# Kernel tuning notes

Measured on AMD Instinct MI355X. Metric: run time of the kernel, lower is better.

The kernel has to match this reference:

```python
import jax, jax.numpy as jnp
import numpy as np

# dims
N_USER = 30000; N_ITEM = 30000; HID = 256; HEADS = 4; DH = HID // HEADS
L = 2; E_BUYS = 200000
IMG_D = 512; TASTE_D = 768; NUTR_D = 20; LR = 64; IMG_RANK = 64
EPS = 1e-5
# node type order: 0=user 1=item 2=taste 3=intention 4=image
# edge type order: taste->item, intention->item, image->item, user->item (buys), item->user (bought_by)


def _bn(x, g, b):
    # nn.BatchNorm1d in training mode (biased variance), deterministic
    mu = jnp.mean(x, axis=0)
    var = jnp.mean((x - mu) ** 2, axis=0)
    return (x - mu) * jax.lax.rsqrt(var + EPS) * g + b


def _segment_softmax(logits, seg, n):
    m = jax.ops.segment_max(logits, seg, num_segments=n)
    m = jnp.where(jnp.isfinite(m), m, 0.0)
    e = jnp.exp(logits - m[seg])
    s = jax.ops.segment_sum(e, seg, num_segments=n)
    return e / (s[seg] + 1e-16)


def _model(p, user_id, item_id, buys_src, buys_dst):
    # --- encoders (dropout = identity in eval) ---
    xu = jax.nn.relu(_bn(p['user_emb'][user_id] @ p['user_W'] + p['user_b'], p['user_bn_g'], p['user_bn_b']))
    xi = jax.nn.relu(_bn(p['item_emb'][item_id] @ p['item_W'] + p['item_b'], p['item_bn_g'], p['item_bn_b']))
    ximg = (p['image_feat'] @ p['img_U']) @ p['img_V'] + p['img_b']  # LowRankLinear
    xt = p['taste_feat'] @ p['taste_W'] + p['taste_b']
    xn = p['intent_feat'] @ p['intent_W'] + p['intent_b']
    xs = [xu, xi, xt, xn, ximg]
    assoc = jnp.arange(N_ITEM, dtype=jnp.int32)
    # (src_type, dst_type, src_idx, dst_idx)
    edges = [(2, 1, assoc, assoc), (3, 1, assoc, assoc), (4, 1, assoc, assoc),
             (0, 1, buys_src, buys_dst), (1, 0, buys_dst, buys_src)]
    scale = 1.0 / np.sqrt(DH)
    n_of = [N_USER, N_ITEM]
    for l in range(L):
        k, q, v = [], [], []
        for t in range(5):
            kqv = xs[t] @ p['kqv_W'][l, t] + p['kqv_b'][l, t]
            kk, qq, vv = jnp.split(kqv, 3, axis=1)
            k.append(kk.reshape(-1, HEADS, DH))
            q.append(qq.reshape(-1, HEADS, DH))
            v.append(vv.reshape(-1, HEADS, DH))
        buf = {0: [], 1: []}
        for e, (s, d, si, di) in enumerate(edges):
            # relation-specific per-head transforms of source k/v (all src nodes, then gather)
            ke = jnp.einsum('nhd,hde->nhe', k[s], p['k_rel'][l, e])
            ve = jnp.einsum('nhd,hde->nhe', v[s], p['v_rel'][l, e])
            logit = jnp.sum(q[d][di] * ke[si], axis=-1) * p['p_rel'][l, e] * scale  # [E,H]
            buf[d].append((logit, ve[si], di))
        new_xs = list(xs)
        for d in (0, 1):  # dst node types: user, item
            logits = jnp.concatenate([b[0] for b in buf[d]], axis=0)
            msgs = jnp.concatenate([b[1] for b in buf[d]], axis=0)
            dsts = jnp.concatenate([b[2] for b in buf[d]], axis=0)
            alpha = _segment_softmax(logits, dsts, n_of[d])  # softmax over ALL incoming edges per dst node
            agg = jax.ops.segment_sum(alpha[:, :, None] * msgs, dsts, num_segments=n_of[d])
            o = jax.nn.gelu(agg.reshape(-1, HID), approximate=False) @ p['out_W'][l, d] + p['out_b'][l, d]
            sg = jax.nn.sigmoid(p['skip'][l, d])
            o = sg * o + (1.0 - sg) * xs[d]  # HGTConv learned skip
            o = o + xs[d]                    # MultiModalFusionGAT residual
            o = jax.nn.relu(_bn(o, p['fbn_g'][l, d], p['fbn_b'][l, d]))  # per-type BN+ReLU (dropout eval)
            new_xs[d] = o
        xs = new_xs  # taste/intention/image pass through unchanged
    return jnp.stack(xs, axis=0)  # [5, 30000, HID]


def setup_inputs():
    key = jax.random.key(0)
    ks = iter(jax.random.split(key, 48))
    def nrm(shape, scale=0.05):
        return jax.random.normal(next(ks), shape, dtype=jnp.float32) * scale
    z = lambda *s: jnp.zeros(s, jnp.float32)
    o = lambda *s: jnp.ones(s, jnp.float32)
    inp = {}
    inp['user_id'] = jnp.arange(N_USER, dtype=jnp.int32)
    inp['item_id'] = jnp.arange(N_ITEM, dtype=jnp.int32)
    inp['buys_src'] = jax.random.randint(next(ks), (E_BUYS,), 0, N_USER, dtype=jnp.int32)
    inp['buys_dst'] = jax.random.randint(next(ks), (E_BUYS,), 0, N_ITEM, dtype=jnp.int32)
    inp['image_feat'] = nrm((N_ITEM, IMG_D), 1.0)
    inp['taste_feat'] = nrm((N_ITEM, TASTE_D), 1.0)
    inp['intent_feat'] = nrm((N_ITEM, NUTR_D), 1.0)
    inp['user_emb'] = nrm((N_USER, LR), 0.1)
    inp['user_W'] = nrm((LR, HID)); inp['user_b'] = z(HID)
    inp['user_bn_g'] = o(HID); inp['user_bn_b'] = z(HID)
    inp['item_emb'] = nrm((N_ITEM, LR), 0.1)
    inp['item_W'] = nrm((LR, HID)); inp['item_b'] = z(HID)
    inp['item_bn_g'] = o(HID); inp['item_bn_b'] = z(HID)
    inp['img_U'] = nrm((IMG_D, IMG_RANK)); inp['img_V'] = nrm((IMG_RANK, HID)); inp['img_b'] = z(HID)
    inp['taste_W'] = nrm((TASTE_D, HID)); inp['taste_b'] = z(HID)
    inp['intent_W'] = nrm((NUTR_D, HID)); inp['intent_b'] = z(HID)
    inp['kqv_W'] = nrm((L, 5, HID, 3 * HID)); inp['kqv_b'] = z(L, 5, 3 * HID)
    inp['out_W'] = nrm((L, 5, HID, HID)); inp['out_b'] = z(L, 5, HID)
    inp['k_rel'] = nrm((L, 5, HEADS, DH, DH))
    inp['v_rel'] = nrm((L, 5, HEADS, DH, DH))
    inp['p_rel'] = o(L, 5, HEADS)
    inp['skip'] = o(L, 5)
    inp['fbn_g'] = o(L, 2, HID); inp['fbn_b'] = z(L, 2, HID)
    return inp


def reference(user_id, item_id, buys_src, buys_dst, image_feat, taste_feat, intent_feat,
              user_emb, user_W, user_b, user_bn_g, user_bn_b,
              item_emb, item_W, item_b, item_bn_g, item_bn_b,
              img_U, img_V, img_b, taste_W, taste_b, intent_W, intent_b,
              kqv_W, kqv_b, out_W, out_b, k_rel, v_rel, p_rel, skip, fbn_g, fbn_b):
    p = dict(image_feat=image_feat, taste_feat=taste_feat, intent_feat=intent_feat,
             user_emb=user_emb, user_W=user_W, user_b=user_b, user_bn_g=user_bn_g, user_bn_b=user_bn_b,
             item_emb=item_emb, item_W=item_W, item_b=item_b, item_bn_g=item_bn_g, item_bn_b=item_bn_b,
             img_U=img_U, img_V=img_V, img_b=img_b, taste_W=taste_W, taste_b=taste_b,
             intent_W=intent_W, intent_b=intent_b, kqv_W=kqv_W, kqv_b=kqv_b, out_W=out_W, out_b=out_b,
             k_rel=k_rel, v_rel=v_rel, p_rel=p_rel, skip=skip, fbn_g=fbn_g, fbn_b=fbn_b)
    return _model(p, user_id, item_id, buys_src, buys_dst)
```

## Files before the change

kernel.cpp:

```cpp
#include <hip/hip_runtime.h>
#include <math.h>

#define HID 256
#define EBUY 200000
#define NNODE 30000
#define MPD 30208
static const size_t S  = (size_t)NNODE * HID;
static const size_t SP = (size_t)MPD * HID;

typedef __attribute__((ext_vector_type(8))) short  short8;
typedef __attribute__((ext_vector_type(4))) float  f32x4;

#define OFF_TASTE 0
#define OFF_INT   196608
#define OFF_IMGU  204800
#define OFF_IMGV  237568
#define OFF_USER  253952
#define OFF_ITEM  270336
#define OFF_OUTW  286720
#define WENC_TOT  548864

__device__ __forceinline__ float gelu_f(float x) {
    return 0.5f * x * (1.0f + erff(x * 0.70710678118654752f));
}
__device__ __forceinline__ unsigned short f2bf(float f) {
    unsigned u = __float_as_uint(f);
    u = (u + 0x7FFFu + ((u >> 16) & 1u)) >> 16;
    return (unsigned short)u;
}
__device__ __forceinline__ float b2f(unsigned short us) {
    return __uint_as_float((unsigned)us << 16);
}
__device__ __forceinline__ void gl_lds16(const unsigned short* g, unsigned short* l) {
    __builtin_amdgcn_global_load_lds(
        (const __attribute__((address_space(1))) unsigned int*)g,
        (__attribute__((address_space(3))) unsigned int*)l, 16, 0, 0);
}
__device__ __forceinline__ int xcd_swz(int bid, int nwg) {
    int q = nwg >> 3, r = nwg & 7;
    int xc = bid & 7, i = bid >> 3;
    int base = (xc < r) ? xc * (q + 1) : r * (q + 1) + (xc - r) * q;
    return base + i;
}

__global__ void conv_pad(const float* __restrict__ in, unsigned short* __restrict__ o,
                         int M, int K, int Kpad)
{
    int i = blockIdx.x * 256 + threadIdx.x;
    if (i >= M * Kpad) return;
    int r = i / Kpad, k = i % Kpad;
    o[i] = (k < K) ? f2bf(in[(size_t)r * K + k]) : (unsigned short)0;
}

__global__ void wtconv_all(const float* __restrict__ taste_W, const float* __restrict__ intent_W,
                           const float* __restrict__ img_U, const float* __restrict__ img_V,
                           const float* __restrict__ user_W, const float* __restrict__ item_W,
                           const float* __restrict__ out_W, unsigned short* __restrict__ WENC)
{
    int i = blockIdx.x * 256 + threadIdx.x;
    if (i >= WENC_TOT) return;
    const float* W; int K, N, Kpad, idx;
    if (i < OFF_INT)        { W = taste_W;  K = 768; N = 256; Kpad = 768; idx = i - OFF_TASTE; }
    else if (i < OFF_IMGU)  { W = intent_W; K = 20;  N = 256; Kpad = 32;  idx = i - OFF_INT; }
    else if (i < OFF_IMGV)  { W = img_U;    K = 512; N = 64;  Kpad = 512; idx = i - OFF_IMGU; }
    else if (i < OFF_USER)  { W = img_V;    K = 64;  N = 256; Kpad = 64;  idx = i - OFF_IMGV; }
    else if (i < OFF_ITEM)  { W = user_W;   K = 64;  N = 256; Kpad = 64;  idx = i - OFF_USER; }
    else if (i < OFF_OUTW)  { W = item_W;   K = 64;  N = 256; Kpad = 64;  idx = i - OFF_ITEM; }
    else {
        int k = (i - OFF_OUTW) >> 16;
        int l = k >> 1, d = k & 1;
        W = out_W + (size_t)(l * 5 + d) * 65536;
        K = 256; N = 256; Kpad = 256; idx = (i - OFF_OUTW) & 65535;
    }
    int n = idx / Kpad, kk = idx % Kpad;
    WENC[i] = (kk < K) ? f2bf(W[(size_t)kk * N + n]) : (unsigned short)0;
}

__global__ void build_kqv(const float* __restrict__ kqv_W, const float* __restrict__ kqv_b,
                          const float* __restrict__ k_rel, const float* __restrict__ v_rel,
                          unsigned short* __restrict__ WALL, float* __restrict__ bALL)
{
    int s = blockIdx.y;
    int l = s / 5, t = s % 5;
    static const int es[5] = {3, 4, 0, 1, 2};
    int e = es[t];
    int tid = blockIdx.x * 256 + threadIdx.x;
    if (tid >= 257 * 768) return;
    int r = tid / 768, c = tid % 768;
    int cb = c >> 8, cc = c & 255;
    int h = cc >> 6, dd = cc & 63;
    const float* W = kqv_W + (size_t)s * 196608;
    const float* bv = kqv_b + (size_t)s * 768;
    const float* Wrow = (r < 256) ? (W + (size_t)r * 768) : bv;
    if (cb == 1) {
        if (t >= 2) return;
        float outv = Wrow[256 + cc];
        if (r < 256) WALL[(size_t)s * 196608 + (size_t)(512 + cc) * 256 + r] = f2bf(outv);
        else         bALL[s * 768 + 512 + cc] = outv;
        return;
    }
    const float* R = ((cb == 0) ? k_rel : v_rel) + (size_t)(l * 5 + e) * 16384 + (size_t)h * 4096;
    int sb = (cb == 0) ? 0 : 512;
    float sum = 0.f;
    #pragma unroll 8
    for (int d = 0; d < 64; ++d)
        sum += Wrow[sb + h * 64 + d] * R[d * 64 + dd];
    int col = (cb == 0) ? cc : 256 + cc;
    if (r < 256) WALL[(size_t)s * 196608 + (size_t)col * 256 + r] = f2bf(sum);
    else         bALL[s * 768 + col] = sum;
}

template<int AF32, int GATH2, int BSEL, int EPI>
__launch_bounds__(256)
__global__ void gemm_mfma(const void* __restrict__ Ap, const void* __restrict__ Ap2,
                          const int* __restrict__ g1, const int* __restrict__ g2,
                          const unsigned short* __restrict__ BT0, int bStride,
                          const float* __restrict__ bias0, const float* __restrict__ bias1,
                          int biasStride,
                          float* __restrict__ D0, unsigned short* __restrict__ Db,
                          unsigned short* __restrict__ Db2,
                          int M, int N, int K)
{
    __shared__ union {
        unsigned short AB[4][4096];
        unsigned short O[16384];
    } sm;
    const int tid = threadIdx.x;
    const int gx = gridDim.x;
    int bid = xcd_swz(blockIdx.y * gx + blockIdx.x, gx * gridDim.y);
    const int bx = bid % gx, by = bid / gx;
    const int row0 = by * 128, col0 = bx * 128;
    const int wid = tid >> 6, lane = tid & 63;
    const int wr = wid >> 1, wc = wid & 1;
    const int l16 = lane & 15, kg = lane >> 4;
    const int tt = (BSEL || GATH2) ? (by / 236) : 0;

    const unsigned short* BT = BT0;
    if (BSEL) BT = BT0 + (size_t)tt * bStride;
    if (GATH2 && tt) BT = BT0 + 16384;
    const float* bias = bias0;
    if (GATH2)              bias = tt ? bias1 : bias0;
    else if (BSEL && bias0) bias = bias0 + (size_t)tt * biasStride;

    f32x4 acc[4][4];
    const f32x4 zero = {0.f, 0.f, 0.f, 0.f};
    #pragma unroll
    for (int i = 0; i < 4; ++i)
        #pragma unroll
        for (int j = 0; j < 4; ++j) acc[i][j] = zero;

    const int lrow = lane >> 2, lchk = lane & 3;
    const int gsw = (lchk ^ ((lrow >> 1) & 3)) * 8;
    int cB0 = min(col0 + wid * 32 + lrow, N - 1);
    int cB1 = min(col0 + wid * 32 + 16 + lrow, N - 1);
    const unsigned short* Bp0 = BT + (size_t)cB0 * K + gsw;
    const unsigned short* Bp1 = BT + (size_t)cB1 * K + gsw;
    const int ofs0 = wid * 1024, ofs1 = wid * 1024 + 512;

    const unsigned short* Ap0b = nullptr; const unsigned short* Ap1b = nullptr;
    const float* Af0 = nullptr; const float* Af1 = nullptr;
    const int rA0 = tid >> 2, rA1 = (tid >> 2) + 64;
    const int q0 = tid & 3;
    const int wsw = (q0 ^ ((rA0 >> 1) & 3)) * 8;
    if (GATH2) {
        int lr0 = row0 + rA0 - tt * MPD; if (lr0 >= NNODE) lr0 = NNODE - 1;
        int lr1 = row0 + rA1 - tt * MPD; if (lr1 >= NNODE) lr1 = NNODE - 1;
        const int* gA = tt ? g2 : g1;
        const float* Abase = tt ? (const float*)Ap2 : (const float*)Ap;
        Af0 = Abase + (size_t)gA[lr0] * K;
        Af1 = Abase + (size_t)gA[lr1] * K;
    } else if (AF32) {
        Af0 = (const float*)Ap + (size_t)min(row0 + rA0, M - 1) * K;
        Af1 = (const float*)Ap + (size_t)min(row0 + rA1, M - 1) * K;
    } else {
        int rr0 = min(row0 + wid * 32 + lrow, M - 1);
        int rr1 = min(row0 + wid * 32 + 16 + lrow, M - 1);
        Ap0b = (const unsigned short*)Ap + (size_t)rr0 * K + gsw;
        Ap1b = (const unsigned short*)Ap + (size_t)rr1 * K + gsw;
    }

    const int nt = K >> 5;
    int cur = 0;
    const int rsw = ((l16 >> 1) & 3);

    #define STAGE_F32(c, k0) do { \
        float4 x0 = *(const float4*)&Af0[(k0) + q0 * 8]; \
        float4 x1 = *(const float4*)&Af0[(k0) + q0 * 8 + 4]; \
        float4 y0 = *(const float4*)&Af1[(k0) + q0 * 8]; \
        float4 y1 = *(const float4*)&Af1[(k0) + q0 * 8 + 4]; \
        ushort4 u0 = {f2bf(x0.x), f2bf(x0.y), f2bf(x0.z), f2bf(x0.w)}; \
        ushort4 u1 = {f2bf(x1.x), f2bf(x1.y), f2bf(x1.z), f2bf(x1.w)}; \
        ushort4 w0 = {f2bf(y0.x), f2bf(y0.y), f2bf(y0.z), f2bf(y0.w)}; \
        ushort4 w1 = {f2bf(y1.x), f2bf(y1.y), f2bf(y1.z), f2bf(y1.w)}; \
        *(ushort4*)&sm.AB[c][rA0 * 32 + wsw]     = u0; \
        *(ushort4*)&sm.AB[c][rA0 * 32 + wsw + 4] = u1; \
        *(ushort4*)&sm.AB[c][rA1 * 32 + wsw]     = w0; \
        *(ushort4*)&sm.AB[c][rA1 * 32 + wsw + 4] = w1; \
        gl_lds16(Bp0 + (k0), &sm.AB[2 + (c)][ofs0]); \
        gl_lds16(Bp1 + (k0), &sm.AB[2 + (c)][ofs1]); \
    } while (0)

    #define STAGE_A(c, k0) do { \
        gl_lds16(Ap0b + (k0), &sm.AB[c][ofs0]); \
        gl_lds16(Ap1b + (k0), &sm.AB[c][ofs1]); \
        gl_lds16(Bp0 + (k0), &sm.AB[2 + (c)][ofs0]); \
        gl_lds16(Bp1 + (k0), &sm.AB[2 + (c)][ofs1]); \
    } while (0)

    #define LOADFRAG(c) do { \
        _Pragma("unroll") \
        for (int i = 0; i < 4; ++i) { \
            af[i]  = *(const short8*)&sm.AB[c][(wr * 64 + i * 16 + l16) * 32 + (kg ^ rsw) * 8]; \
            bfr[i] = *(const short8*)&sm.AB[2 + (c)][(wc * 64 + i * 16 + l16) * 32 + (kg ^ rsw) * 8]; \
        } \
    } while (0)

    #define MMAS() do { \
        _Pragma("unroll") \
        for (int i = 0; i < 4; ++i) \
            _Pragma("unroll") \
            for (int j = 0; j < 4; ++j) \
                acc[i][j] = __builtin_amdgcn_mfma_f32_16x16x32_bf16(af[i], bfr[j], acc[i][j], 0, 0, 0); \
    } while (0)

    if (AF32 || GATH2) {
        STAGE_F32(0, 0);
        __syncthreads();
        for (int s = 0; s < nt; ++s) {
            if (s + 1 < nt) STAGE_F32(cur ^ 1, (s + 1) * 32);
            short8 af[4], bfr[4];
            LOADFRAG(cur);
            MMAS();
            __syncthreads();
            cur ^= 1;
        }
    } else {
        STAGE_A(0, 0);
        for (int s = 0; s < nt; ++s) {
            if (s + 1 < nt) {
                STAGE_A(cur ^ 1, (s + 1) * 32);
                asm volatile("s_waitcnt vmcnt(4)" ::: "memory");
            } else {
                asm volatile("s_waitcnt vmcnt(0)" ::: "memory");
            }
            __builtin_amdgcn_s_barrier();
            asm volatile("" ::: "memory");
            short8 af[4], bfr[4];
            LOADFRAG(cur);
            __builtin_amdgcn_s_setprio(1);
            MMAS();
            __builtin_amdgcn_s_setprio(0);
            __builtin_amdgcn_s_barrier();
            asm volatile("" ::: "memory");
            cur ^= 1;
        }
    }
    #undef STAGE_F32
    #undef STAGE_A
    #undef LOADFRAG
    #undef MMAS

    #pragma unroll
    for (int j = 0; j < 4; ++j) {
        int lc = wc * 64 + j * 16 + l16;
        int cc = col0 + lc;
        float bv = (bias && cc < N) ? bias[cc] : 0.f;
        #pragma unroll
        for (int i = 0; i < 4; ++i) {
            #pragma unroll
            for (int r = 0; r < 4; ++r) {
                int lr = wr * 64 + i * 16 + kg * 4 + r;
                int rr = row0 + lr;
                float v = acc[i][j][r] + bv;
                if (EPI == 0) {
                    if (D0 && cc < N && rr < M) D0[(size_t)rr * N + cc] = v;
                    sm.O[lr * 128 + ((((lc >> 3) ^ (lr & 7)) << 3) | (lc & 7))] = f2bf(v);
                } else if (EPI == 4 || EPI == 5) {
                    sm.O[lr * 128 + ((((lc >> 3) ^ (lr & 7)) << 3) | (lc & 7))] = f2bf(v);
                } else if (EPI == 6) {
                    D0[(size_t)rr * 256 + cc] = v;
                }
            }
        }
    }
    if (EPI == 0 || EPI == 4 || EPI == 5) {
        __syncthreads();
        unsigned short* T; int ldN, cofs;
        if (EPI == 4)      { T = (col0 < 256) ? Db : Db2; ldN = 256; cofs = col0 & 255; }
        else if (EPI == 5) { T = Db; ldN = 256; cofs = col0; }
        else               { T = Db; ldN = N;   cofs = col0; }
        int nloc = N - col0; if (nloc > 128) nloc = 128;
        if (nloc >= 128) {
            int lr = tid >> 1, half = tid & 1;
            int rr = row0 + lr;
            if (EPI != 0 || rr < M) {
                uint4* dst = (uint4*)&T[(size_t)rr * ldN + cofs + half * 64];
                #pragma unroll
                for (int c = 0; c < 8; ++c) {
                    int ch = half * 8 + c;
                    dst[c] = *(const uint4*)&sm.O[lr * 128 + ((ch ^ (lr & 7)) << 3)];
                }
            }
        } else {
            if (tid < 128) {
                int lr = tid, rr = row0 + lr;
                if (rr < M) {
                    uint4* dst = (uint4*)&T[(size_t)rr * ldN + cofs];
                    #pragma unroll
                    for (int c = 0; c < 8; ++c)
                        dst[c] = *(const uint4*)&sm.O[lr * 128 + ((c ^ (lr & 7)) << 3)];
                }
            }
        }
    }
}

__launch_bounds__(256)
__global__ void gemm_outproj(const unsigned short* __restrict__ A,
                             const unsigned short* __restrict__ BT0,
                             const float* __restrict__ bias0,
                             const float* __restrict__ skipB,
                             const float* __restrict__ residB,
                             float* __restrict__ D0, float* __restrict__ bns)
{
    __shared__ unsigned short AB[4][4096];
    const int tid = threadIdx.x;
    int bid = xcd_swz(blockIdx.y * 2 + blockIdx.x, 2 * gridDim.y);
    const int bx = bid % 2, by = bid / 2;
    const int tt = by / 236;
    const int row0 = by * 128, col0 = bx * 128;
    const int row0l = row0 - tt * MPD;
    const int wid = tid >> 6, lane = tid & 63;
    const int wr = wid >> 1, wc = wid & 1;
    const int l16 = lane & 15, kg = lane >> 4;

    const unsigned short* BT = BT0 + (size_t)tt * 65536;
    const float* bias = bias0 + tt * 256;
    const float* resid = residB + (size_t)tt * S;
    float* Dp = D0 + (size_t)tt * SP;
    float* bnp = bns + tt * 512;

    f32x4 acc[4][4];
    const f32x4 zero = {0.f, 0.f, 0.f, 0.f};
    #pragma unroll
    for (int i = 0; i < 4; ++i)
        #pragma unroll
        for (int j = 0; j < 4; ++j) acc[i][j] = zero;

    const int lrow = lane >> 2, lchk = lane & 3;
    const int gsw = (lchk ^ ((lrow >> 1) & 3)) * 8;
    int ar0 = min(row0l + wid * 32 + lrow, NNODE - 1);
    int ar1 = min(row0l + wid * 32 + 16 + lrow, NNODE - 1);
    const unsigned short* Ap0 = A + (size_t)tt * S + (size_t)ar0 * 256 + gsw;
    const unsigned short* Ap1 = A + (size_t)tt * S + (size_t)ar1 * 256 + gsw;
    const unsigned short* Bp0 = BT + (size_t)(col0 + wid * 32 + lrow) * 256 + gsw;
    const unsigned short* Bp1 = BT + (size_t)(col0 + wid * 32 + 16 + lrow) * 256 + gsw;
    const int ofs0 = wid * 1024, ofs1 = wid * 1024 + 512;
    const int rsw = ((l16 >> 1) & 3);
    int cur = 0;

    #define STAGE_O(c, k0) do { \
        gl_lds16(Ap0 + (k0), &AB[c][ofs0]); \
        gl_lds16(Ap1 + (k0), &AB[c][ofs1]); \
        gl_lds16(Bp0 + (k0), &AB[2 + (c)][ofs0]); \
        gl_lds16(Bp1 + (k0), &AB[2 + (c)][ofs1]); \
    } while (0)

    STAGE_O(0, 0);
    for (int s = 0; s < 8; ++s) {
        if (s + 1 < 8) {
            STAGE_O(cur ^ 1, (s + 1) * 32);
            asm volatile("s_waitcnt vmcnt(4)" ::: "memory");
        } else {
            asm volatile("s_waitcnt vmcnt(0)" ::: "memory");
        }
        __builtin_amdgcn_s_barrier();
        asm volatile("" ::: "memory");
        short8 af[4], bfr[4];
        #pragma unroll
        for (int i = 0; i < 4; ++i) {
            af[i]  = *(const short8*)&AB[cur][(wr * 64 + i * 16 + l16) * 32 + (kg ^ rsw) * 8];
            bfr[i] = *(const short8*)&AB[2 + cur][(wc * 64 + i * 16 + l16) * 32 + (kg ^ rsw) * 8];
        }
        __builtin_amdgcn_s_setprio(1);
        #pragma unroll
        for (int i = 0; i < 4; ++i)
            #pragma unroll
            for (int j = 0; j < 4; ++j)
                acc[i][j] = __builtin_amdgcn_mfma_f32_16x16x32_bf16(af[i], bfr[j], acc[i][j], 0, 0, 0);
        __builtin_amdgcn_s_setprio(0);
        __builtin_amdgcn_s_barrier();
        asm volatile("" ::: "memory");
        cur ^= 1;
    }
    #undef STAGE_O

    float sg = 1.f / (1.f + __expf(-skipB[tt]));
    #pragma unroll
    for (int j = 0; j < 4; ++j) {
        int cc = col0 + wc * 64 + j * 16 + l16;
        float cs = 0.f, cs2 = 0.f;
        float bv = bias[cc];
        #pragma unroll
        for (int i = 0; i < 4; ++i) {
            #pragma unroll
            for (int r = 0; r < 4; ++r) {
                int lr = row0l + wr * 64 + i * 16 + kg * 4 + r;
                if (lr < NNODE) {
                    float v = acc[i][j][r] + bv;
                    float xo = resid[(size_t)lr * 256 + cc];
                    float o = sg * v + (2.f - sg) * xo;
                    Dp[(size_t)lr * 256 + cc] = o;
                    cs += o; cs2 += o * o;
                }
            }
        }
        cs  += __shfl_xor(cs, 16);  cs  += __shfl_xor(cs, 32);
        cs2 += __shfl_xor(cs2, 16); cs2 += __shfl_xor(cs2, 32);
        if (kg == 0) {
            atomicAdd(&bnp[cc], cs);
            atomicAdd(&bnp[256 + cc], cs2);
        }
    }
}

__global__ void edge_hist2(const int* __restrict__ dstk, const int* __restrict__ srck,
                           int* __restrict__ cnt)
{
    int j = blockIdx.x * 256 + threadIdx.x;
    if (j < EBUY) atomicAdd(&cnt[dstk[j]], 1);
    else if (j < 2 * EBUY) atomicAdd(&cnt[NNODE + srck[j - EBUY]], 1);
}

#define SCAN_NB 30
#define SCAN_CH 1000
__global__ void scan_part(const int* __restrict__ cnt, int* __restrict__ bt)
{
    int set = blockIdx.y;
    const int* c = cnt + set * NNODE;
    int b = blockIdx.x;
    int i = b * SCAN_CH + threadIdx.x;
    int v = (threadIdx.x < SCAN_CH && i < NNODE) ? c[i] : 0;
    __shared__ int wsum[16];
    int lane = threadIdx.x & 63, wv = threadIdx.x >> 6;
    for (int o = 32; o; o >>= 1) v += __shfl_down(v, o);
    if (lane == 0) wsum[wv] = v;
    __syncthreads();
    if (threadIdx.x == 0) {
        int s = 0;
        for (int w = 0; w < 16; ++w) s += wsum[w];
        bt[set * 32 + b] = s;
    }
}

__global__ void scan_mid(int* __restrict__ bt, int* __restrict__ off_i, int* __restrict__ off_u)
{
    int set = threadIdx.x;
    if (set >= 2) return;
    int* b = bt + set * 32;
    int s = 0;
    for (int i = 0; i < SCAN_NB; ++i) { int c = b[i]; b[i] = s; s += c; }
    (set ? off_u : off_i)[NNODE] = s;
}

__global__ void scan_final(const int* __restrict__ cnt, const int* __restrict__ bt,
                           int* __restrict__ off_i, int* __restrict__ off_u,
                           int* __restrict__ cur_i, int* __restrict__ cur_u)
{
    int set = blockIdx.y;
    const int* c = cnt + set * NNODE;
    int* off = set ? off_u : off_i;
    int* cur = set ? cur_u : cur_i;
    int b = blockIdx.x;
    int i = b * SCAN_CH + threadIdx.x;
    int v = (threadIdx.x < SCAN_CH && i < NNODE) ? c[i] : 0;
    int lane = threadIdx.x & 63, wv = threadIdx.x >> 6;
    int x = v;
    for (int o = 1; o < 64; o <<= 1) { int t = __shfl_up(x, o); if (lane >= o) x += t; }
    __shared__ int wtot[16];
    if (lane == 63) wtot[wv] = x;
    __syncthreads();
    if (wv == 0) {
        int y = (lane < 16) ? wtot[lane] : 0;
        for (int o = 1; o < 16; o <<= 1) { int t = __shfl_up(y, o); if (lane >= o) y += t; }
        if (lane < 16) wtot[lane] = y;
    }
    __syncthreads();
    int wbase = (wv == 0) ? 0 : wtot[wv - 1];
    int excl = bt[set * 32 + b] + wbase + x - v;
    if (threadIdx.x < SCAN_CH && i < NNODE) { off[i] = excl; cur[i] = excl; }
}

__global__ void edge_place2(const int* __restrict__ dstk, const int* __restrict__ srck,
                            int* __restrict__ cur_i, int* __restrict__ cur_u,
                            int* __restrict__ src_i, int* __restrict__ src_u)
{
    int j = blockIdx.x * 256 + threadIdx.x;
    if (j < EBUY) {
        int pos = atomicAdd(&cur_i[dstk[j]], 1);
        src_i[pos] = srck[j];
    } else if (j < 2 * EBUY) {
        int j2 = j - EBUY;
        int pos = atomicAdd(&cur_u[srck[j2]], 1);
        src_u[pos] = dstk[j2];
    }
}

__launch_bounds__(256)
__global__ void attn_both(const unsigned short* __restrict__ QB,
                          const unsigned short* __restrict__ KE,
                          const unsigned short* __restrict__ VE,
                          const int* __restrict__ off_i, const int* __restrict__ src_i,
                          const int* __restrict__ off_u, const int* __restrict__ src_u,
                          const float* __restrict__ pR,
                          unsigned short* __restrict__ AGB)
{
    int gw = (blockIdx.x * 256 + threadIdx.x) >> 6;
    int lane = threadIdx.x & 63;
    if (gw >= 2 * NNODE) return;
    int h = lane >> 4;
    const bool item = gw < NNODE;
    const int wid = item ? gw : gw - NNODE;
    const unsigned short* Qd  = item ? QB + SP : QB;
    const unsigned short* KEs = item ? KE : KE + SP;
    const unsigned short* VEs = item ? VE : VE + SP;
    const int* roff = item ? off_i : off_u;
    const int* srcA = item ? src_i : src_u;
    unsigned short* outp = AGB + (item ? S : 0);

    ushort4 qb = *(const ushort4*)(Qd + (size_t)wid * 256 + lane * 4);
    float4 q = {b2f(qb.x), b2f(qb.y), b2f(qb.z), b2f(qb.w)};
    float m = -INFINITY, s = 0.f;
    float4 acc = {0.f, 0.f, 0.f, 0.f};

    if (item) {
        #pragma unroll
        for (int e = 0; e < 3; ++e) {
            ushort4 kb = *(const ushort4*)(KE + (size_t)(2 + e) * SP + (size_t)wid * 256 + lane * 4);
            float d = q.x * b2f(kb.x) + q.y * b2f(kb.y) + q.z * b2f(kb.z) + q.w * b2f(kb.w);
            for (int off = 8; off; off >>= 1) d += __shfl_xor(d, off, 16);
            float lg = d * pR[e * 4 + h] * 0.125f;
            ushort4 vv = *(const ushort4*)(VE + (size_t)(2 + e) * SP + (size_t)wid * 256 + lane * 4);
            float mn = fmaxf(m, lg);
            float so = __expf(m - mn);
            float ev = __expf(lg - mn);
            s = s * so + ev;
            acc.x = acc.x * so + ev * b2f(vv.x);
            acc.y = acc.y * so + ev * b2f(vv.y);
            acc.z = acc.z * so + ev * b2f(vv.z);
            acc.w = acc.w * so + ev * b2f(vv.w);
            m = mn;
        }
    }

    float pb = pR[(item ? 12 : 16) + h] * 0.125f;
    int j0 = roff[wid], j1 = roff[wid + 1];
    ushort4 kb = {0,0,0,0}, vv = {0,0,0,0};
    if (j0 < j1) {
        int src0 = srcA[j0];
        kb = *(const ushort4*)(KEs + (size_t)src0 * 256 + lane * 4);
        vv = *(const ushort4*)(VEs + (size_t)src0 * 256 + lane * 4);
    }
    for (int j = j0; j < j1; ++j) {
        ushort4 ckb = kb, cvv = vv;
        if (j + 1 < j1) {
            int ns = srcA[j + 1];
            kb = *(const ushort4*)(KEs + (size_t)ns * 256 + lane * 4);
            vv = *(const ushort4*)(VEs + (size_t)ns * 256 + lane * 4);
        }
        float d = q.x * b2f(ckb.x) + q.y * b2f(ckb.y) + q.z * b2f(ckb.z) + q.w * b2f(ckb.w);
        for (int off = 8; off; off >>= 1) d += __shfl_xor(d, off, 16);
        float lg = d * pb;
        float mn = fmaxf(m, lg);
        float so = __expf(m - mn);
        float ev = __expf(lg - mn);
        s = s * so + ev;
        acc.x = acc.x * so + ev * b2f(cvv.x);
        acc.y = acc.y * so + ev * b2f(cvv.y);
        acc.z = acc.z * so + ev * b2f(cvv.z);
        acc.w = acc.w * so + ev * b2f(cvv.w);
        m = mn;
    }

    float inv = 1.f / (s + 1e-16f);
    ushort4 o4;
    o4.x = f2bf(gelu_f(acc.x * inv));
    o4.y = f2bf(gelu_f(acc.y * inv));
    o4.z = f2bf(gelu_f(acc.z * inv));
    o4.w = f2bf(gelu_f(acc.w * inv));
    *(ushort4*)(outp + (size_t)wid * 256 + lane * 4) = o4;
}

#define BNB 512
__global__ void bn_stats2(const float* __restrict__ SCRf, float* __restrict__ part)
{
    int tt = blockIdx.y;
    const float* x = SCRf + (size_t)tt * SP;
    int col = threadIdx.x;
    int b = blockIdx.x;
    float s = 0.f, s2 = 0.f;
    int r = b;
    for (; r + 3 * BNB < NNODE; r += 4 * BNB) {
        float v0 = x[(size_t)r * 256 + col];
        float v1 = x[(size_t)(r + BNB) * 256 + col];
        float v2 = x[(size_t)(r + 2 * BNB) * 256 + col];
        float v3 = x[(size_t)(r + 3 * BNB) * 256 + col];
        s += v0 + v1 + v2 + v3;
        s2 += v0 * v0 + v1 * v1 + v2 * v2 + v3 * v3;
    }
    for (; r < NNODE; r += BNB) {
        float v = x[(size_t)r * 256 + col];
        s += v; s2 += v * v;
    }
    part[((size_t)tt * BNB + b) * 512 + col] = s;
    part[((size_t)tt * BNB + b) * 512 + 256 + col] = s2;
}

__global__ void bn_fin2(const float* __restrict__ part,
                        const float* __restrict__ g0, const float* __restrict__ b0,
                        const float* __restrict__ g1, const float* __restrict__ b1,
                        float* __restrict__ scsh)
{
    int tid = threadIdx.x;
    int tt = tid >> 8, col = tid & 255;
    const float* p = part + (size_t)tt * BNB * 512;
    float s = 0.f, s2 = 0.f;
    #pragma unroll 4
    for (int b = 0; b < BNB; ++b) { s += p[b * 512 + col]; s2 += p[b * 512 + 256 + col]; }
    float mu = s / (float)NNODE;
    float var = s2 / (float)NNODE - mu * mu;
    float sc = rsqrtf(var + 1e-5f) * (tt ? g1 : g0)[col];
    scsh[tt * 512 + col] = sc;
    scsh[tt * 512 + 256 + col] = (tt ? b1 : b0)[col] - mu * sc;
}

__global__ void bn_find2(const float* __restrict__ bns,
                         const float* __restrict__ g01, const float* __restrict__ b01,
                         float* __restrict__ scsh)
{
    int tid = threadIdx.x;
    int tt = tid >> 8, col = tid & 255;
    float s = bns[tt * 512 + col], s2 = bns[tt * 512 + 256 + col];
    float mu = s / (float)NNODE;
    float var = s2 / (float)NNODE - mu * mu;
    float sc = rsqrtf(var + 1e-5f) * g01[tt * 256 + col];
    scsh[tt * 512 + col] = sc;
    scsh[tt * 512 + 256 + col] = b01[tt * 256 + col] - mu * sc;
}

__global__ void bn_apply2(const float* __restrict__ SCRf, const float* __restrict__ scsh,
                          float* __restrict__ out, unsigned short* __restrict__ XBall)
{
    const int Q4 = NNODE * 64;
    for (int i = blockIdx.x * 256 + threadIdx.x; i < 2 * Q4; i += gridDim.x * 256) {
        int tt = (i >= Q4) ? 1 : 0;
        int local = i - tt * Q4;
        int c4 = local & 63;
        float4 sc4 = *(const float4*)&scsh[tt * 512 + c4 * 4];
        float4 sh4 = *(const float4*)&scsh[tt * 512 + 256 + c4 * 4];
        float4 v = ((const float4*)(SCRf + (size_t)tt * SP))[local];
        v.x = fmaxf(v.x * sc4.x + sh4.x, 0.f);
        v.y = fmaxf(v.y * sc4.y + sh4.y, 0.f);
        v.z = fmaxf(v.z * sc4.z + sh4.z, 0.f);
        v.w = fmaxf(v.w * sc4.w + sh4.w, 0.f);
        ((float4*)(out + (size_t)tt * S))[local] = v;
        ushort4 u = {f2bf(v.x), f2bf(v.y), f2bf(v.z), f2bf(v.w)};
        ((ushort4*)(XBall + (size_t)tt * SP))[local] = u;
    }
}

extern "C" void kernel_launch(void* const* d_in, const int* in_sizes, int n_in,
                              void* d_out, int out_size, void* d_ws, size_t ws_size,
                              hipStream_t stream)
{
    const int*   user_id    = (const int*)d_in[0];
    const int*   item_id    = (const int*)d_in[1];
    const int*   buys_src   = (const int*)d_in[2];
    const int*   buys_dst   = (const int*)d_in[3];
    const float* image_feat = (const float*)d_in[4];
    const float* taste_feat = (const float*)d_in[5];
    const float* intent_feat= (const float*)d_in[6];
    const float* user_emb   = (const float*)d_in[7];
    const float* user_W     = (const float*)d_in[8];
    const float* user_b     = (const float*)d_in[9];
    const float* user_bn_g  = (const float*)d_in[10];
    const float* user_bn_b  = (const float*)d_in[11];
    const float* item_emb   = (const float*)d_in[12];
    const float* item_W     = (const float*)d_in[13];
    const float* item_b     = (const float*)d_in[14];
    const float* item_bn_g  = (const float*)d_in[15];
    const float* item_bn_b  = (const float*)d_in[16];
    const float* img_U      = (const float*)d_in[17];
    const float* img_V      = (const float*)d_in[18];
    const float* img_b      = (const float*)d_in[19];
    const float* taste_W    = (const float*)d_in[20];
    const float* taste_b    = (const float*)d_in[21];
    const float* intent_W   = (const float*)d_in[22];
    const float* intent_b   = (const float*)d_in[23];
    const float* kqv_W      = (const float*)d_in[24];
    const float* kqv_b      = (const float*)d_in[25];
    const float* out_W      = (const float*)d_in[26];
    const float* out_b      = (const float*)d_in[27];
    const float* k_rel      = (const float*)d_in[28];
    const float* v_rel      = (const float*)d_in[29];
    const float* p_rel      = (const float*)d_in[30];
    const float* skip       = (const float*)d_in[31];
    const float* fbn_g      = (const float*)d_in[32];
    const float* fbn_b      = (const float*)d_in[33];

    float* out = (float*)d_out;
    float* ws  = (float*)d_ws;

    float* SCRf = ws;
    float* BNSp = SCRf + 2 * SP;
    float* BNS  = BNSp + 2 * BNB * 512;
    float* SCSH = BNS + 1024;
    float* bALL = SCSH + 1024;
    unsigned short* QB    = (unsigned short*)(bALL + 7680);
    unsigned short* XBall = QB + 2 * SP;
    unsigned short* KEall = XBall + 5 * SP;
    unsigned short* VEall = KEall + 5 * SP;
    unsigned short* AGB   = VEall + 5 * SP;
    unsigned short* IMB   = AGB + 2 * S;
    unsigned short* IPB   = IMB + (size_t)NNODE * 64;
    unsigned short* WALL  = IPB + (size_t)NNODE * 32;
    unsigned short* WENC  = WALL + (size_t)10 * 196608;
    int* cnt   = (int*)(WENC + WENC_TOT);
    int* off_i = cnt + 2 * NNODE;
    int* off_u = off_i + NNODE + 1;
    int* cur_i = off_u + NNODE + 1;
    int* cur_u = cur_i + NNODE;
    int* src_i = cur_u + NNODE;
    int* src_u = src_i + EBUY;
    int* bt    = src_u + EBUY;

    size_t need = (size_t)((char*)(bt + 64) - (char*)ws);
    if (ws_size < need) return;

    hipMemsetAsync(cnt, 0, 2 * NNODE * 4, stream);
    edge_hist2<<<(2 * EBUY + 255) / 256, 256, 0, stream>>>(buys_dst, buys_src, cnt);
    scan_part<<<dim3(SCAN_NB, 2), 1024, 0, stream>>>(cnt, bt);
    scan_mid<<<1, 64, 0, stream>>>(bt, off_i, off_u);
    scan_final<<<dim3(SCAN_NB, 2), 1024, 0, stream>>>(cnt, bt, off_i, off_u, cur_i, cur_u);
    edge_place2<<<(2 * EBUY + 255) / 256, 256, 0, stream>>>(buys_dst, buys_src, cur_i, cur_u, src_i, src_u);

    wtconv_all<<<(WENC_TOT + 255) / 256, 256, 0, stream>>>(taste_W, intent_W, img_U, img_V,
                                                           user_W, item_W, out_W, WENC);
    build_kqv<<<dim3(771, 10), 256, 0, stream>>>(kqv_W, kqv_b, k_rel, v_rel, WALL, bALL);
    conv_pad<<<(NNODE * 32 + 255) / 256, 256, 0, stream>>>(intent_feat, IPB, NNODE, 20, 32);

    hipLaunchKernelGGL((gemm_mfma<1,0,0,0>), dim3(2,235), dim3(256), 0, stream,
        taste_feat, nullptr, nullptr, nullptr, WENC + OFF_TASTE, 0, taste_b, nullptr, 0,
        out + 2*S, XBall + 2*SP, nullptr, NNODE, 256, 768);
    hipLaunchKernelGGL((gemm_mfma<0,0,0,0>), dim3(2,235), dim3(256), 0, stream,
        IPB, nullptr, nullptr, nullptr, WENC + OFF_INT, 0, intent_b, nullptr, 0,
        out + 3*S, XBall + 3*SP, nullptr, NNODE, 256, 32);
    hipLaunchKernelGGL((gemm_mfma<1,0,0,0>), dim3(1,235), dim3(256), 0, stream,
        image_feat, nullptr, nullptr, nullptr, WENC + OFF_IMGU, 0, nullptr, nullptr, 0,
        nullptr, IMB, nullptr, NNODE, 64, 512);
    hipLaunchKernelGGL((gemm_mfma<0,0,0,0>), dim3(2,235), dim3(256), 0, stream,
        IMB, nullptr, nullptr, nullptr, WENC + OFF_IMGV, 0, img_b, nullptr, 0,
        out + 4*S, XBall + 4*SP, nullptr, NNODE, 256, 64);
    hipLaunchKernelGGL((gemm_mfma<1,1,0,6>), dim3(2,472), dim3(256), 0, stream,
        user_emb, item_emb, user_id, item_id, WENC + OFF_USER, 0, user_b, item_b, 0,
        SCRf, nullptr, nullptr, 2*MPD, 256, 64);
    bn_stats2<<<dim3(BNB, 2), 256, 0, stream>>>(SCRf, BNSp);
    bn_fin2<<<1, 512, 0, stream>>>(BNSp, user_bn_g, user_bn_b, item_bn_g, item_bn_b, SCSH);
    bn_apply2<<<960, 256, 0, stream>>>(SCRf, SCSH, out, XBall);

    for (int l = 0; l < 2; ++l) {
        hipLaunchKernelGGL((gemm_mfma<0,0,1,4>), dim3(4, 5*236), dim3(256), 0, stream,
            XBall, nullptr, nullptr, nullptr, WALL + (size_t)l*5*196608, 196608,
            bALL + l*5*768, nullptr, 768, nullptr, KEall, VEall,
            5*MPD, 512, 256);
        hipLaunchKernelGGL((gemm_mfma<0,0,1,5>), dim3(2, 2*236), dim3(256), 0, stream,
            XBall, nullptr, nullptr, nullptr, WALL + (size_t)l*5*196608 + 512*256, 196608,
            bALL + l*5*768 + 512, nullptr, 768, nullptr, QB, nullptr,
            2*MPD, 256, 256);
        hipLaunchKernelGGL(attn_both, dim3((2*NNODE*64 + 255)/256), dim3(256), 0, stream,
            QB, KEall, VEall, off_i, src_i, off_u, src_u, p_rel + l*20, AGB);
        hipMemsetAsync(BNS, 0, 1024 * 4, stream);
        hipLaunchKernelGGL(gemm_outproj, dim3(2, 472), dim3(256), 0, stream,
            AGB, WENC + OFF_OUTW + (size_t)l*2*65536, out_b + (size_t)l*5*256,
            skip + l*5, out, SCRf, BNS);
        bn_find2<<<1, 512, 0, stream>>>(BNS, fbn_g + (size_t)l*2*256, fbn_b + (size_t)l*2*256, SCSH);
        bn_apply2<<<960, 256, 0, stream>>>(SCRf, SCSH, out, XBall);
    }
}
```

Before: 993.2 us.

## Fuse K/V/Q projection GEMMs into one launch and pre-convert fp32 features to bf16

Replaces the separate KV and Q projection GEMM launches in each layer with a single specialised kernel over a flattened grid. Node types 0-1 get K, V and Q tiles, types 2-4 get only K and V. The kernel has a fixed-K double-buffered MFMA loop and writes each 128-column tile straight to the KE, VE or QB buffer. Taste and image features are also converted to bf16 once by a vectorised kernel, so the encoder GEMMs can use the bf16 A path instead of converting fp32 on the fly. The cost is an extra conversion pass and its memory traffic, and scratch buffers (SCRf, QB) are reused for the converted features, which depends on their lifetimes not overlapping.

```diff
diff --git a/kernel.cpp b/kernel.cpp
--- a/kernel.cpp
+++ b/kernel.cpp
@@ -50,6 +50,24 @@
     if (i >= M * Kpad) return;
     int r = i / Kpad, k = i % Kpad;
     o[i] = (k < K) ? f2bf(in[(size_t)r * K + k]) : (unsigned short)0;
+}
+
+__global__ void conv2bf(const float* __restrict__ a, int na4, unsigned short* __restrict__ oa,
+                        const float* __restrict__ b, int nb4, unsigned short* __restrict__ ob)
+{
+    int total = na4 + nb4;
+    for (int i = blockIdx.x * 256 + threadIdx.x; i < total; i += gridDim.x * 256) {
+        if (i < na4) {
+            float4 v = ((const float4*)a)[i];
+            ushort4 u = {f2bf(v.x), f2bf(v.y), f2bf(v.z), f2bf(v.w)};
+            ((ushort4*)oa)[i] = u;
+        } else {
+            int j = i - na4;
+            float4 v = ((const float4*)b)[j];
+            ushort4 u = {f2bf(v.x), f2bf(v.y), f2bf(v.z), f2bf(v.w)};
+            ((ushort4*)ob)[j] = u;
+        }
+    }
 }
 
 __global__ void wtconv_all(const float* __restrict__ taste_W, const float* __restrict__ intent_W,
@@ -110,15 +128,13 @@
     else         bALL[s * 768 + col] = sum;
 }
 
-template<int AF32, int GATH2, int BSEL, int EPI>
+template<int AF32, int GATH2, int EPI>
 __launch_bounds__(256)
 __global__ void gemm_mfma(const void* __restrict__ Ap, const void* __restrict__ Ap2,
                           const int* __restrict__ g1, const int* __restrict__ g2,
-                          const unsigned short* __restrict__ BT0, int bStride,
+                          const unsigned short* __restrict__ BT0,
                           const float* __restrict__ bias0, const float* __restrict__ bias1,
-                          int biasStride,
                           float* __restrict__ D0, unsigned short* __restrict__ Db,
-                          unsigned short* __restrict__ Db2,
                           int M, int N, int K)
 {
     __shared__ union {
@@ -133,14 +149,12 @@
     const int wid = tid >> 6, lane = tid & 63;
     const int wr = wid >> 1, wc = wid & 1;
     const int l16 = lane & 15, kg = lane >> 4;
-    const int tt = (BSEL || GATH2) ? (by / 236) : 0;
+    const int tt = GATH2 ? (by / 236) : 0;
 
     const unsigned short* BT = BT0;
-    if (BSEL) BT = BT0 + (size_t)tt * bStride;
     if (GATH2 && tt) BT = BT0 + 16384;
     const float* bias = bias0;
-    if (GATH2)              bias = tt ? bias1 : bias0;
-    else if (BSEL && bias0) bias = bias0 + (size_t)tt * biasStride;
+    if (GATH2) bias = tt ? bias1 : bias0;
 
     f32x4 acc[4][4];
     const f32x4 zero = {0.f, 0.f, 0.f, 0.f};
@@ -275,26 +289,20 @@
                 if (EPI == 0) {
                     if (D0 && cc < N && rr < M) D0[(size_t)rr * N + cc] = v;
                     sm.O[lr * 128 + ((((lc >> 3) ^ (lr & 7)) << 3) | (lc & 7))] = f2bf(v);
-                } else if (EPI == 4 || EPI == 5) {
-                    sm.O[lr * 128 + ((((lc >> 3) ^ (lr & 7)) << 3) | (lc & 7))] = f2bf(v);
                 } else if (EPI == 6) {
                     D0[(size_t)rr * 256 + cc] = v;
                 }
             }
         }
     }
-    if (EPI == 0 || EPI == 4 || EPI == 5) {
+    if (EPI == 0) {
         __syncthreads();
-        unsigned short* T; int ldN, cofs;
-        if (EPI == 4)      { T = (col0 < 256) ? Db : Db2; ldN = 256; cofs = col0 & 255; }
-        else if (EPI == 5) { T = Db; ldN = 256; cofs = col0; }
-        else               { T = Db; ldN = N;   cofs = col0; }
         int nloc = N - col0; if (nloc > 128) nloc = 128;
         if (nloc >= 128) {
             int lr = tid >> 1, half = tid & 1;
             int rr = row0 + lr;
-            if (EPI != 0 || rr < M) {
-                uint4* dst = (uint4*)&T[(size_t)rr * ldN + cofs + half * 64];
+            if (rr < M) {
+                uint4* dst = (uint4*)&Db[(size_t)rr * N + col0 + half * 64];
                 #pragma unroll
                 for (int c = 0; c < 8; ++c) {
                     int ch = half * 8 + c;
@@ -305,12 +313,121 @@
             if (tid < 128) {
                 int lr = tid, rr = row0 + lr;
                 if (rr < M) {
-                    uint4* dst = (uint4*)&T[(size_t)rr * ldN + cofs];
+                    uint4* dst = (uint4*)&Db[(size_t)rr * N + col0];
                     #pragma unroll
                     for (int c = 0; c < 8; ++c)
                         dst[c] = *(const uint4*)&sm.O[lr * 128 + ((c ^ (lr & 7)) << 3)];
                 }
             }
+        }
+    }
+}
+
+__launch_bounds__(256)
+__global__ void gemm_kvq768(const unsigned short* __restrict__ A,
+                            const unsigned short* __restrict__ WALLl,
+                            const float* __restrict__ bALLl,
+                            unsigned short* __restrict__ KE,
+                            unsigned short* __restrict__ VE,
+                            unsigned short* __restrict__ QB)
+{
+    __shared__ union {
+        unsigned short AB[4][4096];
+        unsigned short O[16384];
+    } sm;
+    const int tid = threadIdx.x;
+    int f = xcd_swz(blockIdx.x, 5664);
+    int tt, bx, by;
+    if (f < 2832) { tt = f / 1416; int r = f % 1416; bx = r / 236; by = r % 236; }
+    else          { int g = f - 2832; tt = 2 + g / 944; int r = g % 944; bx = r / 236; by = r % 236; }
+    const int row0 = by * 128, col0 = bx * 128;
+    const int wid = tid >> 6, lane = tid & 63;
+    const int wr = wid >> 1, wc = wid & 1;
+    const int l16 = lane & 15, kg = lane >> 4;
+
+    const unsigned short* Ab = A + (size_t)tt * SP;
+    const unsigned short* BT = WALLl + (size_t)tt * 196608;
+    const float* bias = bALLl + tt * 768;
+
+    f32x4 acc[4][4];
+    const f32x4 zero = {0.f, 0.f, 0.f, 0.f};
+    #pragma unroll
+    for (int i = 0; i < 4; ++i)
+        #pragma unroll
+        for (int j = 0; j < 4; ++j) acc[i][j] = zero;
+
+    const int lrow = lane >> 2, lchk = lane & 3;
+    const int gsw = (lchk ^ ((lrow >> 1) & 3)) * 8;
+    const unsigned short* Ap0 = Ab + (size_t)(row0 + wid * 32 + lrow) * 256 + gsw;
+    const unsigned short* Ap1 = Ab + (size_t)(row0 + wid * 32 + 16 + lrow) * 256 + gsw;
+    const unsigned short* Bp0 = BT + (size_t)(col0 + wid * 32 + lrow) * 256 + gsw;
+    const unsigned short* Bp1 = BT + (size_t)(col0 + wid * 32 + 16 + lrow) * 256 + gsw;
+    const int ofs0 = wid * 1024, ofs1 = wid * 1024 + 512;
+    const int rsw = ((l16 >> 1) & 3);
+    int cur = 0;
+
+    #define STAGE_K(c, k0) do { \
+        gl_lds16(Ap0 + (k0), &sm.AB[c][ofs0]); \
+        gl_lds16(Ap1 + (k0), &sm.AB[c][ofs1]); \
+        gl_lds16(Bp0 + (k0), &sm.AB[2 + (c)][ofs0]); \
+        gl_lds16(Bp1 + (k0), &sm.AB[2 + (c)][ofs1]); \
+    } while (0)
+
+    STAGE_K(0, 0);
+    for (int s = 0; s < 8; ++s) {
+        if (s + 1 < 8) {
+            STAGE_K(cur ^ 1, (s + 1) * 32);
+            asm volatile("s_waitcnt vmcnt(4)" ::: "memory");
+        } else {
+            asm volatile("s_waitcnt vmcnt(0)" ::: "memory");
+        }
+        __builtin_amdgcn_s_barrier();
+        asm volatile("" ::: "memory");
+        short8 af[4], bfr[4];
+        #pragma unroll
+        for (int i = 0; i < 4; ++i) {
+            af[i]  = *(const short8*)&sm.AB[cur][(wr * 64 + i * 16 + l16) * 32 + (kg ^ rsw) * 8];
+            bfr[i] = *(const short8*)&sm.AB[2 + cur][(wc * 64 + i * 16 + l16) * 32 + (kg ^ rsw) * 8];
+        }
+        __builtin_amdgcn_s_setprio(1);
+        #pragma unroll
+        for (int i = 0; i < 4; ++i)
+            #pragma unroll
+            for (int j = 0; j < 4; ++j)
+                acc[i][j] = __builtin_amdgcn_mfma_f32_16x16x32_bf16(af[i], bfr[j], acc[i][j], 0, 0, 0);
+        __builtin_amdgcn_s_setprio(0);
+        __builtin_amdgcn_s_barrier();
+        asm volatile("" ::: "memory");
+        cur ^= 1;
+    }
+    #undef STAGE_K
+
+    #pragma unroll
+    for (int j = 0; j < 4; ++j) {
+        int lc = wc * 64 + j * 16 + l16;
+        float bv = bias[col0 + lc];
+        #pragma unroll
+        for (int i = 0; i < 4; ++i) {
+            #pragma unroll
+            for (int r = 0; r < 4; ++r) {
+                int lr = wr * 64 + i * 16 + kg * 4 + r;
+                float v = acc[i][j][r] + bv;
+                sm.O[lr * 128 + ((((lc >> 3) ^ (lr & 7)) << 3) | (lc & 7))] = f2bf(v);
+            }
+        }
+    }
+    __syncthreads();
+    {
+        int dsel = bx >> 1;
+        unsigned short* T = ((dsel == 0) ? KE : (dsel == 1) ? VE : QB) + (size_t)tt * SP;
+        int cofs = (bx & 1) * 128;
+        int lr = tid >> 1, half = tid & 1;
+        int rr = row0 + lr;
+        uint4* dst = (uint4*)&T[(size_t)rr * 256 + cofs + half * 64];
+        #pragma unroll
+        for (int c = 0; c < 8; ++c) {
+            int ch = half * 8 + c;
+            dst[c] = *(const uint4*)&sm.O[lr * 128 + ((ch ^ (lr & 7)) << 3)];
         }
     }
 }
@@ -737,6 +854,9 @@
     size_t need = (size_t)((char*)(bt + 64) - (char*)ws);
     if (ws_size < need) return;
 
+    unsigned short* TFB = (unsigned short*)SCRf;
+    unsigned short* IFB = QB;
+
     hipMemsetAsync(cnt, 0, 2 * NNODE * 4, stream);
     edge_hist2<<<(2 * EBUY + 255) / 256, 256, 0, stream>>>(buys_dst, buys_src, cnt);
     scan_part<<<dim3(SCAN_NB, 2), 1024, 0, stream>>>(cnt, bt);
@@ -748,35 +868,30 @@
                                                            user_W, item_W, out_W, WENC);
     build_kqv<<<dim3(771, 10), 256, 0, stream>>>(kqv_W, kqv_b, k_rel, v_rel, WALL, bALL);
     conv_pad<<<(NNODE * 32 + 255) / 256, 256, 0, stream>>>(intent_feat, IPB, NNODE, 20, 32);
-
-    hipLaunchKernelGGL((gemm_mfma<1,0,0,0>), dim3(2,235), dim3(256), 0, stream,
-        taste_feat, nullptr, nullptr, nullptr, WENC + OFF_TASTE, 0, taste_b, nullptr, 0,
-        out + 2*S, XBall + 2*SP, nullptr, NNODE, 256, 768);
-    hipLaunchKernelGGL((gemm_mfma<0,0,0,0>), dim3(2,235), dim3(256), 0, stream,
-        IPB, nullptr, nullptr, nullptr, WENC + OFF_INT, 0, intent_b, nullptr, 0,
-        out + 3*S, XBall + 3*SP, nullptr, NNODE, 256, 32);
-    hipLaunchKernelGGL((gemm_mfma<1,0,0,0>), dim3(1,235), dim3(256), 0, stream,
-        image_feat, nullptr, nullptr, nullptr, WENC + OFF_IMGU, 0, nullptr, nullptr, 0,
-        nullptr, IMB, nullptr, NNODE, 64, 512);
-    hipLaunchKernelGGL((gemm_mfma<0,0,0,0>), dim3(2,235), dim3(256), 0, stream,
-        IMB, nullptr, nullptr, nullptr, WENC + OFF_IMGV, 0, img_b, nullptr, 0,
-        out + 4*S, XBall + 4*SP, nullptr, NNODE, 256, 64);
-    hipLaunchKernelGGL((gemm_mfma<1,1,0,6>), dim3(2,472), dim3(256), 0, stream,
-        user_emb, item_emb, user_id, item_id, WENC + OFF_USER, 0, user_b, item_b, 0,
-        SCRf, nullptr, nullptr, 2*MPD, 256, 64);
+    conv2bf<<<2048, 256, 0, stream>>>(taste_feat, 5760000, TFB, image_feat, 3840000, IFB);
+
+    hipLaunchKernelGGL((gemm_mfma<0,0,0>), dim3(2,235), dim3(256), 0, stream,
+        TFB, nullptr, nullptr, nullptr, WENC + OFF_TASTE, taste_b, nullptr,
+        out + 2*S, XBall + 2*SP, NNODE, 256, 768);
+    hipLaunchKernelGGL((gemm_mfma<0,0,0>), dim3(2,235), dim3(256), 0, stream,
+        IPB, nullptr, nullptr, nullptr, WENC + OFF_INT, intent_b, nullptr,
+        out + 3*S, XBall + 3*SP, NNODE, 256, 32);
+    hipLaunchKernelGGL((gemm_mfma<0,0,0>), dim3(1,235), dim3(256), 0, stream,
+        IFB, nullptr, nullptr, nullptr, WENC + OFF_IMGU, nullptr, nullptr,
+        nullptr, IMB, NNODE, 64, 512);
+    hipLaunchKernelGGL((gemm_mfma<0,0,0>), dim3(2,235), dim3(256), 0, stream,
+        IMB, nullptr, nullptr, nullptr, WENC + OFF_IMGV, img_b, nullptr,
+        out + 4*S, XBall + 4*SP, NNODE, 256, 64);
+    hipLaunchKernelGGL((gemm_mfma<1,1,6>), dim3(2,472), dim3(256), 0, stream,
+        user_emb, item_emb, user_id, item_id, WENC + OFF_USER, user_b, item_b,
+        SCRf, nullptr, 2*MPD, 256, 64);
     bn_stats2<<<dim3(BNB, 2), 256, 0, stream>>>(SCRf, BNSp);
     bn_fin2<<<1, 512, 0, stream>>>(BNSp, user_bn_g, user_bn_b, item_bn_g, item_bn_b, SCSH);
     bn_apply2<<<960, 256, 0, stream>>>(SCRf, SCSH, out, XBall);
 
     for (int l = 0; l < 2; ++l) {
-        hipLaunchKernelGGL((gemm_mfma<0,0,1,4>), dim3(4, 5*236), dim3(256), 0, stream,
-            XBall, nullptr, nullptr, nullptr, WALL + (size_t)l*5*196608, 196608,
-            bALL + l*5*768, nullptr, 768, nullptr, KEall, VEall,
-            5*MPD, 512, 256);
-        hipLaunchKernelGGL((gemm_mfma<0,0,1,5>), dim3(2, 2*236), dim3(256), 0, stream,
-            XBall, nullptr, nullptr, nullptr, WALL + (size_t)l*5*196608 + 512*256, 196608,
-            bALL + l*5*768 + 512, nullptr, 768, nullptr, QB, nullptr,
-            2*MPD, 256, 256);
+        hipLaunchKernelGGL(gemm_kvq768, dim3(5664), dim3(256), 0, stream,
+            XBall, WALL + (size_t)l*5*196608, bALL + l*5*768, KEall, VEall, QB);
         hipLaunchKernelGGL(attn_both, dim3((2*NNODE*64 + 255)/256), dim3(256), 0, stream,
             QB, KEall, VEall, off_i, src_i, off_u, src_u, p_rel + l*20, AGB);
         hipMemsetAsync(BNS, 0, 1024 * 4, stream);
```

New measurement: 958.0 us. -3.6%, faster.
